# Kernel tuning notes

Measured on AMD Instinct MI355X. Metric: run time of the kernel, lower is better.

The kernel has to match this reference:

```python
import jax, jax.numpy as jnp
import numpy as np

B = 65536
DIM = 256       # latent_dim
N_EMBED = 1024  # codebook size


def setup_inputs() -> dict:
    key = jax.random.key(0)
    kx, ke = jax.random.split(key)
    x = jax.random.normal(kx, (B, DIM), dtype=jnp.float32)
    # rosinality Quantize stores codebook as embed[dim, n_embed]
    embed = jax.random.normal(ke, (DIM, N_EMBED), dtype=jnp.float32)
    return {"x": x, "embed": embed}


def reference(x, embed):
    # dist[b, k] = ||x_b||^2 - 2 x_b . e_k + ||e_k||^2  (negated for argmax in
    # the original; equivalent to argmin of the distance)
    x_sq = jnp.sum(x * x, axis=1, keepdims=True)            # [B, 1]
    e_sq = jnp.sum(embed * embed, axis=0, keepdims=True)    # [1, K]
    dist = x_sq - 2.0 * (x @ embed) + e_sq                  # [B, K]
    embed_ind = jnp.argmin(dist, axis=1)                    # [B] int
    # codebook lookup: embed.T is [K, dim]
    quantize = jnp.take(embed.T, embed_ind, axis=0)         # [B, dim]
    # commitment loss term
    diff = jnp.mean(jnp.square(jax.lax.stop_gradient(quantize) - x))
    # straight-through estimator
    quantize_st = x + jax.lax.stop_gradient(quantize - x)
    return quantize_st, diff, embed_ind
```

## Files before the change

### kernel.cpp

```cpp
#include <hip/hip_runtime.h>

#define NROWSQ   65536
#define NDIM     256
#define NCB      1024
#define DIFF_OFF 16777216
#define IDX_OFF  16777217

#define MARGIN_A 0.35f
#define MARGIN_B 1.5e-3f
#define SCORE_SHIFT 384.0f

typedef __attribute__((ext_vector_type(8))) short s16x8;
typedef __attribute__((ext_vector_type(4))) float f32x4;

__device__ __forceinline__ unsigned short f2bf(float f) {
  union { float f; unsigned u; } v; v.f = f;
  return (unsigned short)((v.u + 0x7FFFu + ((v.u >> 16) & 1u)) >> 16);
}

__device__ __forceinline__ void top2_update(float& v1, int& i1, float& v2, int& i2,
                                            float v, int col) {
  if (v > v1 || (v == v1 && col < i1)) { v2 = v1; i2 = i1; v1 = v; i1 = col; }
  else if (v > v2 || (v == v2 && col < i2)) { v2 = v; i2 = col; }
}
__device__ __forceinline__ void top2_merge(float& v1, int& i1, float& v2, int& i2,
                                           float ov1, int oi1, float ov2, int oi2) {
  if (ov1 > v1 || (ov1 == v1 && oi1 < i1)) {
    float nv2 = v1; int ni2 = i1;
    if (ov2 > nv2 || (ov2 == nv2 && oi2 < ni2)) { nv2 = ov2; ni2 = oi2; }
    v1 = ov1; i1 = oi1; v2 = nv2; i2 = ni2;
  } else if (ov1 > v2 || (ov1 == v2 && oi1 < i2)) {
    v2 = ov1; i2 = oi1;
  }
}

__device__ __forceinline__ float np_pairwise128(const float* p) {
  float r0 = p[0], r1 = p[1], r2 = p[2], r3 = p[3];
  float r4 = p[4], r5 = p[5], r6 = p[6], r7 = p[7];
  for (int i = 8; i < 128; i += 8) {
    r0 += p[i];     r1 += p[i + 1]; r2 += p[i + 2]; r3 += p[i + 3];
    r4 += p[i + 4]; r5 += p[i + 5]; r6 += p[i + 6]; r7 += p[i + 7];
  }
  return ((r0 + r1) + (r2 + r3)) + ((r4 + r5) + (r6 + r7));
}

__global__ void k0a_transpose(const float* __restrict__ E, float* __restrict__ embT,
                              unsigned short* __restrict__ cbT,
                              int* __restrict__ cntA, int* __restrict__ cntB) {
  __shared__ float T[64][65];
  const int t = threadIdx.x;
  const int kbase = (blockIdx.x & 15) * 64;
  const int dbase = (blockIdx.x >> 4) * 64;
  if (blockIdx.x == 0 && t == 0) { *cntA = 0; *cntB = 0; }
  #pragma unroll
  for (int i = 0; i < 4; ++i) {
    const int cid = i * 256 + t;
    const int dl = cid >> 4, kc = cid & 15;
    const float4 v = *(const float4*)(E + (size_t)(dbase + dl) * NCB + kbase + kc * 4);
    T[dl][kc * 4 + 0] = v.x; T[dl][kc * 4 + 1] = v.y;
    T[dl][kc * 4 + 2] = v.z; T[dl][kc * 4 + 3] = v.w;
  }
  __syncthreads();
  #pragma unroll
  for (int i = 0; i < 4; ++i) {
    const int cid = i * 256 + t;
    const int kl = cid >> 4, dc = cid & 15;
    float4 v;
    v.x = T[dc * 4 + 0][kl]; v.y = T[dc * 4 + 1][kl];
    v.z = T[dc * 4 + 2][kl]; v.w = T[dc * 4 + 3][kl];
    *(float4*)(embT + (size_t)(kbase + kl) * NDIM + dbase + dc * 4) = v;
    ushort4 b;
    b.x = f2bf(v.x); b.y = f2bf(v.y); b.z = f2bf(v.z); b.w = f2bf(v.w);
    *(ushort4*)(cbT + (size_t)(kbase + kl) * NDIM + dbase + dc * 4) = b;
  }
}

__global__ void k0b_esq(const float* __restrict__ embT, float* __restrict__ esq32,
                        float* __restrict__ esqs, float* __restrict__ esqr) {
  const int b = blockIdx.x, t = threadIdx.x;
  if (b < 128) {
    const int col = b * 8 + (t >> 5);
    const int l = t & 31;
    double s = 0.0;
    #pragma unroll
    for (int i = 0; i < 8; ++i) {
      const double v = (double)embT[(size_t)col * NDIM + l + i * 32];
      s += v * v;
    }
    #pragma unroll
    for (int m = 16; m >= 1; m >>= 1) s += __shfl_xor(s, m);
    if (l == 0) {
      esq32[col] = (float)(0.5 * s);
      esqs[col] = (float)(0.5 * s) - SCORE_SHIFT;
    }
  } else {
    const int col = (b - 128) * 256 + t;
    float sr = 0.f;
    for (int d = 0; d < NDIM; ++d) {
      const float v = embT[(size_t)col * NDIM + d];
      sr = sr + v * v;
    }
    esqr[col] = sr;
  }
}

#define BLD 264

__global__ void k1_scores(
    const float* __restrict__ X, const unsigned short* __restrict__ cbT,
    const float* __restrict__ esqs, int2* __restrict__ part1) {
  __shared__ __align__(16) unsigned short Bs[64 * BLD];
  __shared__ float esq_l[1024];
  const int t = threadIdx.x;
  const int lane = t & 63, w = t >> 6;
  const int l15 = lane & 15, quad = lane >> 4;
  const int rowbase = blockIdx.x * 128;

  {
    const float4 e4 = *(const float4*)(esqs + t * 4);
    *(float4*)(esq_l + t * 4) = e4;
  }

  s16x8 afrag[2][8];
  #pragma unroll
  for (int m = 0; m < 2; ++m) {
    const float* xr = X + (size_t)(rowbase + w * 32 + m * 16 + l15) * NDIM;
    #pragma unroll
    for (int ks = 0; ks < 8; ++ks) {
      const float4 xa = *(const float4*)(xr + ks * 32 + quad * 8);
      const float4 xb = *(const float4*)(xr + ks * 32 + quad * 8 + 4);
      s16x8 a;
      a[0] = (short)f2bf(xa.x); a[1] = (short)f2bf(xa.y);
      a[2] = (short)f2bf(xa.z); a[3] = (short)f2bf(xa.w);
      a[4] = (short)f2bf(xb.x); a[5] = (short)f2bf(xb.y);
      a[6] = (short)f2bf(xb.z); a[7] = (short)f2bf(xb.w);
      afrag[m][ks] = a;
    }
  }

  int key1[2][4], key2[2][4];
  #pragma unroll
  for (int m = 0; m < 2; ++m)
    #pragma unroll
    for (int r = 0; r < 4; ++r) { key1[m][r] = 0; key2[m][r] = 0; }

  for (int nt = 0; nt < 16; ++nt) {
    __syncthreads();
    #pragma unroll
    for (int i = 0; i < 8; ++i) {
      const int id = i * 256 + t;
      const int c = id >> 5, d8 = id & 31;
      *(uint4*)&Bs[c * BLD + d8 * 8] =
          *(const uint4*)(cbT + (size_t)(nt * 64 + c) * NDIM + d8 * 8);
    }
    __syncthreads();

    f32x4 acc[2][4];
    #pragma unroll
    for (int m = 0; m < 2; ++m)
      #pragma unroll
      for (int s = 0; s < 4; ++s) acc[m][s] = (f32x4){0.f, 0.f, 0.f, 0.f};

    #pragma unroll
    for (int ks = 0; ks < 8; ++ks) {
      #pragma unroll
      for (int s = 0; s < 4; ++s) {
        const s16x8 b = *(const s16x8*)&Bs[(s * 16 + l15) * BLD + ks * 32 + quad * 8];
        acc[0][s] = __builtin_amdgcn_mfma_f32_16x16x32_bf16(afrag[0][ks], b, acc[0][s], 0, 0, 0);
        acc[1][s] = __builtin_amdgcn_mfma_f32_16x16x32_bf16(afrag[1][ks], b, acc[1][s], 0, 0, 0);
      }
    }

    #pragma unroll
    for (int s = 0; s < 4; ++s) {
      const int lcol = nt * 64 + s * 16 + l15;
      const float eq = esq_l[lcol];
      const int suffix = 1023 - lcol;
      #pragma unroll
      for (int m = 0; m < 2; ++m)
        #pragma unroll
        for (int r = 0; r < 4; ++r) {
          float sc = acc[m][s][r] - eq;
          sc = fmaxf(sc, 1.0f);
          const int key = (__float_as_int(sc) & 0xFFFFFC00) | suffix;
          key2[m][r] = max(key2[m][r], min(key1[m][r], key));
          key1[m][r] = max(key1[m][r], key);
        }
    }
  }

  #pragma unroll
  for (int mask = 1; mask <= 8; mask <<= 1) {
    #pragma unroll
    for (int m = 0; m < 2; ++m)
      #pragma unroll
      for (int r = 0; r < 4; ++r) {
        const int ok1 = __shfl_xor(key1[m][r], mask);
        const int ok2 = __shfl_xor(key2[m][r], mask);
        const int n1 = max(key1[m][r], ok1);
        const int n2 = max(min(key1[m][r], ok1), max(key2[m][r], ok2));
        key1[m][r] = n1; key2[m][r] = n2;
      }
  }

  if (l15 == 0) {
    #pragma unroll
    for (int m = 0; m < 2; ++m)
      #pragma unroll
      for (int r = 0; r < 4; ++r) {
        const int grow = rowbase + w * 32 + m * 16 + quad * 4 + r;
        part1[grow] = make_int2(key1[m][r], key2[m][r]);
      }
  }
}

__global__ void k1m_merge(const int2* __restrict__ part1, float* __restrict__ outIdx,
                          int* __restrict__ cntA, int* __restrict__ listA,
                          float* __restrict__ outDiff) {
  const int row = blockIdx.x * 256 + threadIdx.x;
  if (row == 0) *outDiff = 0.f;
  const int2 a = part1[row];
  outIdx[row] = (float)(1023 - (a.x & 1023));
  const float g1 = __int_as_float(a.x & 0xFFFFFC00);
  const float g2 = __int_as_float(a.y & 0xFFFFFC00);
  if (g1 - g2 < MARGIN_A) {
    const int p = atomicAdd(cntA, 1);
    listA[p] = row;
  }
}

__global__ __launch_bounds__(256) void k2a_refine(
    const float* __restrict__ X, const float* __restrict__ E,
    const float* __restrict__ esq, const int* __restrict__ cntA,
    const int* __restrict__ listA, float4* __restrict__ part2) {
  __shared__ float Xs[8][NDIM];
  __shared__ float rv1[4][8], rv2[4][8];
  __shared__ int   ri1[4][8], ri2[4][8];
  const int t = threadIdx.x;
  const int lane = t & 63, w = t >> 6;
  const int half = blockIdx.x & 1;
  const int bstride = gridDim.x >> 1;
  const int cnt = *cntA;
  const int k0 = half * 512 + t * 2;
  for (int base = (blockIdx.x >> 1) * 8; base < cnt; base += bstride * 8) {
    const int nrows = min(8, cnt - base);
    __syncthreads();
    for (int r = 0; r < 8; ++r) {
      const int rid = listA[base + min(r, nrows - 1)];
      Xs[r][t] = X[(size_t)rid * NDIM + t];
    }
    __syncthreads();

    float acc[8][2];
    #pragma unroll
    for (int r = 0; r < 8; ++r) { acc[r][0] = 0.f; acc[r][1] = 0.f; }

    for (int d = 0; d < NDIM; ++d) {
      const float2 e = *(const float2*)(E + d * NCB + k0);
      #pragma unroll
      for (int r = 0; r < 8; ++r) {
        const float x = Xs[r][d];
        acc[r][0] += x * e.x; acc[r][1] += x * e.y;
      }
    }
    const float eq0 = esq[k0], eq1 = esq[k0 + 1];

    #pragma unroll
    for (int r = 0; r < 8; ++r) {
      float bv1 = -3.4e38f, bv2 = -3.4e38f; int bi1 = 0x7fffffff, bi2 = 0x7fffffff;
      top2_update(bv1, bi1, bv2, bi2, acc[r][0] - eq0, k0);
      top2_update(bv1, bi1, bv2, bi2, acc[r][1] - eq1, k0 + 1);
      #pragma unroll
      for (int mask = 1; mask < 64; mask <<= 1) {
        const float ov1 = __shfl_xor(bv1, mask); const int oi1 = __shfl_xor(bi1, mask);
        const float ov2 = __shfl_xor(bv2, mask); const int oi2 = __shfl_xor(bi2, mask);
        top2_merge(bv1, bi1, bv2, bi2, ov1, oi1, ov2, oi2);
      }
      if (lane == 0) { rv1[w][r] = bv1; ri1[w][r] = bi1; rv2[w][r] = bv2; ri2[w][r] = bi2; }
    }
    __syncthreads();
    if (t < nrows) {
      const int r = t;
      float fv1 = rv1[0][r], fv2 = rv2[0][r]; int fi1 = ri1[0][r], fi2 = ri2[0][r];
      for (int ww = 1; ww < 4; ++ww)
        top2_merge(fv1, fi1, fv2, fi2, rv1[ww][r], ri1[ww][r], rv2[ww][r], ri2[ww][r]);
      part2[half * NROWSQ + base + r] = make_float4(fv1, (float)fi1, fv2, (float)fi2);
    }
    __syncthreads();
  }
}

__global__ void k2m_merge(const float4* __restrict__ part2, const int* __restrict__ cntA,
                          const int* __restrict__ listA, float* __restrict__ outIdx,
                          int* __restrict__ cntB, int* __restrict__ listB) {
  const int cnt = *cntA;
  for (int j = blockIdx.x * 256 + threadIdx.x; j < cnt; j += gridDim.x * 256) {
    const float4 a = part2[j];
    const float4 b = part2[NROWSQ + j];
    float v1 = a.x, v2 = a.z; int i1 = (int)a.y, i2 = (int)a.w;
    top2_merge(v1, i1, v2, i2, b.x, (int)b.y, b.z, (int)b.w);
    const int rid = listA[j];
    outIdx[rid] = (float)i1;
    if (v1 - v2 < MARGIN_B) { const int p = atomicAdd(cntB, 1); listB[p] = rid; }
  }
}

__global__ __launch_bounds__(256) void k2b_mimic(
    const float* __restrict__ X, const float* __restrict__ embT,
    const float* __restrict__ esqr, const int* __restrict__ cntB,
    const int* __restrict__ listB, float* __restrict__ outIdx) {
  __shared__ float Xr[NDIM];
  __shared__ float Psq[NDIM];
  __shared__ float rv[256];
  __shared__ int ri[256];
  const int t = threadIdx.x;
  const int cnt = *cntB;
  for (int j = blockIdx.x; j < cnt; j += gridDim.x) {
    const int rid = listB[j];
    __syncthreads();
    {
      const float x = X[(size_t)rid * NDIM + t];
      Xr[t] = x;
      Psq[t] = x * x;
    }
    __syncthreads();
    const float x_sq = np_pairwise128(Psq) + np_pairwise128(Psq + 128);

    float best = 3.4e38f; int bidx = 0x7fffffff;
    #pragma unroll
    for (int c = 0; c < 4; ++c) {
      const int k = t + c * 256;
      const float* er = embT + (size_t)k * NDIM;
      float acc = 0.f;
      #pragma unroll 8
      for (int dq = 0; dq < 64; ++dq) {
        const float4 e = *(const float4*)(er + dq * 4);
        const float4 x = *(const float4*)(Xr + dq * 4);
        acc = fmaf(x.x, e.x, acc);
        acc = fmaf(x.y, e.y, acc);
        acc = fmaf(x.z, e.z, acc);
        acc = fmaf(x.w, e.w, acc);
      }
      const float dist = (x_sq - 2.0f * acc) + esqr[k];
      if (dist < best || (dist == best && k < bidx)) { best = dist; bidx = k; }
    }
    rv[t] = best; ri[t] = bidx;
    __syncthreads();
    for (int off = 128; off > 0; off >>= 1) {
      if (t < off) {
        if (rv[t + off] < rv[t] || (rv[t + off] == rv[t] && ri[t + off] < ri[t])) {
          rv[t] = rv[t + off]; ri[t] = ri[t + off];
        }
      }
      __syncthreads();
    }
    if (t == 0) outIdx[rid] = (float)ri[0];
  }
}

__global__ __launch_bounds__(256) void k4_outputs(
    const float* __restrict__ X, const float* __restrict__ embT,
    const float* __restrict__ idxF, float* __restrict__ outQ,
    float* __restrict__ outDiff) {
  const int t = threadIdx.x;
  const int lane = t & 63, w = t >> 6;
  const int W = blockIdx.x * 4 + w;
  float s = 0.f;
  #pragma unroll
  for (int i = 0; i < 8; ++i) {
    const int r = W + i * 8192;
    const int idx = (int)idxF[r];
    const float4 q = *(const float4*)(embT + idx * NDIM + lane * 4);
    const float4 x = *(const float4*)(X + (size_t)r * NDIM + lane * 4);
    *(float4*)(outQ + (size_t)r * NDIM + lane * 4) = q;
    const float dx = q.x - x.x, dy = q.y - x.y, dz = q.z - x.z, dw = q.w - x.w;
    s += dx * dx + dy * dy + dz * dz + dw * dw;
  }
  #pragma unroll
  for (int mask = 1; mask < 64; mask <<= 1) s += __shfl_xor(s, mask);
  __shared__ float bs[4];
  if (lane == 0) bs[w] = s;
  __syncthreads();
  if (t == 0)
    atomicAdd(outDiff, (bs[0] + bs[1] + bs[2] + bs[3]) * (1.0f / 16777216.0f));
}

extern "C" void kernel_launch(void* const* d_in, const int* in_sizes, int n_in,
                              void* d_out, int out_size, void* d_ws, size_t ws_size,
                              hipStream_t stream) {
  const float* X = (const float*)d_in[0];
  const float* E = (const float*)d_in[1];
  float* out = (float*)d_out;

  char* ws = (char*)d_ws;
  unsigned short* cbT = (unsigned short*)(ws + 0x000000);
  float*  embT  = (float*) (ws + 0x080000);
  float*  esq32 = (float*) (ws + 0x180000);
  float*  esqs  = (float*) (ws + 0x181000);
  float*  esqr  = (float*) (ws + 0x182000);
  int* cntA  = (int*)(ws + 0x183000);
  int* cntB  = (int*)(ws + 0x183004);
  int* listA = (int*)(ws + 0x183100);
  int* listB = (int*)(ws + 0x1C3100);
  int2*   part1 = (int2*)  (ws + 0x203100);
  float4* part2 = (float4*)(ws + 0x303100);

  float* outQ    = out;
  float* outDiff = out + DIFF_OFF;
  float* outIdx  = out + IDX_OFF;

  k0a_transpose<<<dim3(64), dim3(256), 0, stream>>>(E, embT, cbT, cntA, cntB);
  k0b_esq<<<dim3(132), dim3(256), 0, stream>>>(embT, esq32, esqs, esqr);
  k1_scores<<<dim3(512), dim3(256), 0, stream>>>(X, cbT, esqs, part1);
  k1m_merge<<<dim3(256), dim3(256), 0, stream>>>(part1, outIdx, cntA, listA, outDiff);
  k2a_refine<<<dim3(1024), dim3(256), 0, stream>>>(X, E, esq32, cntA, listA, part2);
  k2m_merge<<<dim3(64), dim3(256), 0, stream>>>(part2, cntA, listA, outIdx, cntB, listB);
  k2b_mimic<<<dim3(64), dim3(256), 0, stream>>>(X, embT, esqr, cntB, listB, outIdx);
  k4_outputs<<<dim3(2048), dim3(256), 0, stream>>>(X, embT, outIdx, outQ, outDiff);
}
```

Before: 345.3 us.

## Double-buffer codebook tiles via direct global-to-LDS loads with XOR swizzle

The scores kernel now stages each 64-code bf16 tile with global_load_lds into a double buffer, prefetching the next tile while MFMAs run on the current one. This replaces the synchronous register round-trip and the padded layout. Bank conflicts are avoided by an XOR swizzle, which the transpose kernel applies when it writes the bf16 codebook. Separately, the per-code fp32 squared-norm pass is spread over 64 blocks that stage rows in LDS, replacing 4 blocks that read strided global memory. The cost is double the LDS footprint, which may lower occupancy, plus a full vmcnt wait and barrier every iteration.

```diff
diff --git a/kernel.cpp b/kernel.cpp
--- a/kernel.cpp
+++ b/kernel.cpp
@@ -16,6 +16,12 @@
 __device__ __forceinline__ unsigned short f2bf(float f) {
   union { float f; unsigned u; } v; v.f = f;
   return (unsigned short)((v.u + 0x7FFFu + ((v.u >> 16) & 1u)) >> 16);
+}
+
+__device__ __forceinline__ void gll16(const void* g, void* l) {
+  __builtin_amdgcn_global_load_lds(
+      (const __attribute__((address_space(1))) unsigned int*)g,
+      (__attribute__((address_space(3))) unsigned int*)l, 16, 0, 0);
 }
 
 __device__ __forceinline__ void top2_update(float& v1, int& i1, float& v2, int& i2,
@@ -71,7 +77,9 @@
     *(float4*)(embT + (size_t)(kbase + kl) * NDIM + dbase + dc * 4) = v;
     ushort4 b;
     b.x = f2bf(v.x); b.y = f2bf(v.y); b.z = f2bf(v.z); b.w = f2bf(v.w);
-    *(ushort4*)(cbT + (size_t)(kbase + kl) * NDIM + dbase + dc * 4) = b;
+    const int dcol = dbase + dc * 4;
+    const int sp = dcol ^ ((kl & 7) << 3);
+    *(ushort4*)(cbT + (size_t)(kbase + kl) * NDIM + sp) = b;
   }
 }
 
@@ -94,32 +102,41 @@
       esqs[col] = (float)(0.5 * s) - SCORE_SHIFT;
     }
   } else {
-    const int col = (b - 128) * 256 + t;
-    float sr = 0.f;
-    for (int d = 0; d < NDIM; ++d) {
-      const float v = embT[(size_t)col * NDIM + d];
-      sr = sr + v * v;
-    }
-    esqr[col] = sr;
-  }
-}
-
-#define BLD 264
+    __shared__ float Ls[16][260];
+    const int col0 = (b - 128) * 16;
+    #pragma unroll
+    for (int i = 0; i < 4; ++i) {
+      const int flat = i * 256 + t;
+      const int row = flat >> 6, f4 = flat & 63;
+      *(float4*)&Ls[row][f4 * 4] =
+          *(const float4*)(embT + (size_t)(col0 + row) * NDIM + f4 * 4);
+    }
+    __syncthreads();
+    if (t < 16) {
+      float sr = 0.f;
+      for (int d = 0; d < NDIM; ++d) {
+        const float v = Ls[t][d];
+        sr = sr + v * v;
+      }
+      esqr[col0 + t] = sr;
+    }
+  }
+}
 
 __global__ void k1_scores(
     const float* __restrict__ X, const unsigned short* __restrict__ cbT,
     const float* __restrict__ esqs, int2* __restrict__ part1) {
-  __shared__ __align__(16) unsigned short Bs[64 * BLD];
+  __shared__ __align__(16) unsigned short Bs[2][64 * 256];
   __shared__ float esq_l[1024];
   const int t = threadIdx.x;
   const int lane = t & 63, w = t >> 6;
   const int l15 = lane & 15, quad = lane >> 4;
   const int rowbase = blockIdx.x * 128;
-
-  {
-    const float4 e4 = *(const float4*)(esqs + t * 4);
-    *(float4*)(esq_l + t * 4) = e4;
-  }
+  const int swz = (l15 & 7) << 3;
+
+  #pragma unroll
+  for (int i = 0; i < 8; ++i)
+    gll16(cbT + (size_t)(i * 256 + t) * 8, &Bs[0][(i * 256 + w * 64) * 8]);
 
   s16x8 afrag[2][8];
   #pragma unroll
@@ -138,22 +155,28 @@
     }
   }
 
+  {
+    const float4 e4 = *(const float4*)(esqs + t * 4);
+    *(float4*)(esq_l + t * 4) = e4;
+  }
+
   int key1[2][4], key2[2][4];
   #pragma unroll
   for (int m = 0; m < 2; ++m)
     #pragma unroll
     for (int r = 0; r < 4; ++r) { key1[m][r] = 0; key2[m][r] = 0; }
 
+  asm volatile("s_waitcnt vmcnt(0)" ::: "memory");
+  __syncthreads();
+
+  int cur = 0;
   for (int nt = 0; nt < 16; ++nt) {
-    __syncthreads();
-    #pragma unroll
-    for (int i = 0; i < 8; ++i) {
-      const int id = i * 256 + t;
-      const int c = id >> 5, d8 = id & 31;
-      *(uint4*)&Bs[c * BLD + d8 * 8] =
-          *(const uint4*)(cbT + (size_t)(nt * 64 + c) * NDIM + d8 * 8);
-    }
-    __syncthreads();
+    if (nt < 15) {
+      const unsigned short* src = cbT + (size_t)(nt + 1) * (64 * 256);
+      #pragma unroll
+      for (int i = 0; i < 8; ++i)
+        gll16(src + (size_t)(i * 256 + t) * 8, &Bs[cur ^ 1][(i * 256 + w * 64) * 8]);
+    }
 
     f32x4 acc[2][4];
     #pragma unroll
@@ -165,9 +188,10 @@
     for (int ks = 0; ks < 8; ++ks) {
       #pragma unroll
       for (int s = 0; s < 4; ++s) {
-        const s16x8 b = *(const s16x8*)&Bs[(s * 16 + l15) * BLD + ks * 32 + quad * 8];
-        acc[0][s] = __builtin_amdgcn_mfma_f32_16x16x32_bf16(afrag[0][ks], b, acc[0][s], 0, 0, 0);
-        acc[1][s] = __builtin_amdgcn_mfma_f32_16x16x32_bf16(afrag[1][ks], b, acc[1][s], 0, 0, 0);
+        const int us = (s * 16 + l15) * 256 + ((ks * 32 + quad * 8) ^ swz);
+        const s16x8 bfr = *(const s16x8*)&Bs[cur][us];
+        acc[0][s] = __builtin_amdgcn_mfma_f32_16x16x32_bf16(afrag[0][ks], bfr, acc[0][s], 0, 0, 0);
+        acc[1][s] = __builtin_amdgcn_mfma_f32_16x16x32_bf16(afrag[1][ks], bfr, acc[1][s], 0, 0, 0);
       }
     }
 
@@ -187,6 +211,10 @@
           key1[m][r] = max(key1[m][r], key);
         }
     }
+
+    asm volatile("s_waitcnt vmcnt(0)" ::: "memory");
+    __syncthreads();
+    cur ^= 1;
   }
 
   #pragma unroll
@@ -410,7 +438,7 @@
   float* outIdx  = out + IDX_OFF;
 
   k0a_transpose<<<dim3(64), dim3(256), 0, stream>>>(E, embT, cbT, cntA, cntB);
-  k0b_esq<<<dim3(132), dim3(256), 0, stream>>>(embT, esq32, esqs, esqr);
+  k0b_esq<<<dim3(192), dim3(256), 0, stream>>>(embT, esq32, esqs, esqr);
   k1_scores<<<dim3(512), dim3(256), 0, stream>>>(X, cbT, esqs, part1);
   k1m_merge<<<dim3(256), dim3(256), 0, stream>>>(part1, outIdx, cntA, listA, outDiff);
   k2a_refine<<<dim3(1024), dim3(256), 0, stream>>>(X, E, esq32, cntA, listA, part2);
```

Result: faster. 319.4 us (-7.5%).
